# Optimization experiments

Measured on AMD Instinct MI355X. Metric: run time of the kernel, lower is better.

The kernel has to match this reference:

```python
import jax, jax.numpy as jnp
import numpy as np


def _conv2d(x, w, pad):
    return jax.lax.conv_general_dilated(
        x, w, (1, 1), [(pad, pad), (pad, pad)],
        dimension_numbers=('NCHW', 'OIHW', 'NCHW'))


def _affine_grid(theta, k):
    # torch F.affine_grid, align_corners=False; output size (k, k)
    base = ((2.0 * jnp.arange(k) + 1.0) / k - 1.0).astype(jnp.float32)
    pts = jnp.stack([
        jnp.broadcast_to(base[None, :], (k, k)),  # x varies along width
        jnp.broadcast_to(base[:, None], (k, k)),  # y varies along height
        jnp.ones((k, k), jnp.float32)], -1)        # [k,k,3]
    return jnp.einsum('ijc,nrc->nijr', pts, theta)  # [N,k,k,2] -> (x,y)


def _grid_sample(img, grid):
    # torch F.grid_sample: bilinear, zeros padding, align_corners=False
    # img [C,H,W], grid [k,k,2] with (x,y) in [-1,1]
    C, H, W = img.shape
    gx = (grid[..., 0] + 1.0) * W * 0.5 - 0.5
    gy = (grid[..., 1] + 1.0) * H * 0.5 - 0.5
    x0 = jnp.floor(gx); y0 = jnp.floor(gy)
    wx = gx - x0; wy = gy - y0
    x0i = x0.astype(jnp.int32); y0i = y0.astype(jnp.int32)

    def gath(yi, xi):
        valid = ((xi >= 0) & (xi < W) & (yi >= 0) & (yi < H)).astype(img.dtype)
        v = img[:, jnp.clip(yi, 0, H - 1), jnp.clip(xi, 0, W - 1)]  # [C,k,k]
        return v * valid[None]

    v00 = gath(y0i, x0i); v01 = gath(y0i, x0i + 1)
    v10 = gath(y0i + 1, x0i); v11 = gath(y0i + 1, x0i + 1)
    return (v00 * ((1 - wx) * (1 - wy))[None] + v01 * (wx * (1 - wy))[None]
            + v10 * ((1 - wx) * wy)[None] + v11 * (wx * wy)[None])


def reference(x, stn0_w, stn0_b, stn1_w, lin_w, lin_b, check):
    B, C, H, W = x.shape
    k = stn1_w.shape[-1]
    h = jax.nn.relu(_conv2d(x, stn0_w, k // 2) + stn0_b[None, :, None, None])
    ident6 = jnp.array([1., 0., 0., 0., 1., 0.], jnp.float32)
    out = _conv2d(h, stn1_w, 0) * (1.0 - check) + ident6[None, :, None, None]
    Ho, Wo = out.shape[2], out.shape[3]
    N = B * Ho * Wo
    # permute(0,3,2,1).view(N,2,3) as in torch
    theta = out.transpose(0, 3, 2, 1).reshape(N, 2, 3)
    grid = _affine_grid(theta, k)  # [N,k,k,2]
    xv = jnp.arange(k // 2, k // 2 + Ho, dtype=jnp.float32)[:, None]  # meshgrid 'ij'
    yv = jnp.arange(k // 2, k // 2 + Wo, dtype=jnp.float32)[None, :]
    half = float(k // 2)
    auxx = ((grid[..., 0] * half).reshape(B, Ho, Wo, k, k)
            + xv[None, :, :, None, None]).reshape(N, k, k) / (H - 1) * 2.0 - 1.0
    auxy = ((grid[..., 1] * half).reshape(B, Ho, Wo, k, k)
            + yv[None, :, :, None, None]).reshape(N, k, k) / (W - 1) * 2.0 - 1.0
    auxgrid = jnp.stack([auxx, auxy], -1).reshape(B, Ho * Wo, k, k, 2)
    # tile(x,0,Ho*Wo) duplicates x[b] for each of its Ho*Wo grids; gather directly
    xs = jax.vmap(lambda img, g: jax.vmap(lambda gg: _grid_sample(img, gg))(g))(x, auxgrid)  # [B,P,C,k,k]
    x_out = xs.reshape(N, -1) @ lin_w.T + lin_b  # [N,O]
    score = x_out.reshape(B, Ho, Wo, -1).transpose(0, 3, 2, 1)  # [B,O,Wo,Ho] as in torch
    ident23 = jnp.array([[1., 0., 0.], [0., 1., 0.]], jnp.float32)
    return score, ident23[None] - theta, out, auxx, auxy


def setup_inputs() -> dict:
    key = jax.random.key(0)
    ks = jax.random.split(key, 6)
    C, O, k = 128, 256, 3
    B, H, W = 8, 56, 56
    x = jax.random.normal(ks[0], (B, C, H, W), jnp.float32)
    stn0_w = jax.random.normal(ks[1], (C, C, k, k), jnp.float32) * (1.0 / np.sqrt(C * k * k))
    stn0_b = jax.random.normal(ks[2], (C,), jnp.float32) * 0.01
    # original zero-inits stn1; use small random so theta is non-trivial
    stn1_w = jax.random.normal(ks[3], (6, C, k, k), jnp.float32) * 0.01
    lin_w = jax.random.normal(ks[4], (O, C * k * k), jnp.float32) * (1.0 / np.sqrt(C * k * k))
    lin_b = jax.random.normal(ks[5], (O,), jnp.float32) * 0.01
    return {'x': x, 'stn0_w': stn0_w, 'stn0_b': stn0_b, 'stn1_w': stn1_w,
            'lin_w': lin_w, 'lin_b': lin_b, 'check': 0}
```

## Files before the change

kernel.cpp:

```cpp
#include <hip/hip_runtime.h>

typedef __attribute__((ext_vector_type(4))) float f32x4;
typedef __attribute__((ext_vector_type(8))) short bf16x8;

#define OPLANE 2916
#define NN 23328
#define KDIM 1152
#define PLANE 3136
#define LDP 72

__device__ __forceinline__ unsigned short f2bf(float f) {
    unsigned u = __builtin_bit_cast(unsigned, f);
    u += 0x7fffu + ((u >> 16) & 1u);
    return (unsigned short)(u >> 16);
}
__device__ __forceinline__ float bflo(unsigned u) {
    return __builtin_bit_cast(float, u << 16);
}
__device__ __forceinline__ float bfhi(unsigned u) {
    return __builtin_bit_cast(float, u & 0xffff0000u);
}

__global__ __launch_bounds__(256) void k_pre(const float* __restrict__ x,
                                             const float* __restrict__ w0,
                                             const float* __restrict__ lw,
                                             unsigned short* __restrict__ xnh,
                                             unsigned short* __restrict__ b1t,
                                             unsigned short* __restrict__ b2t) {
    __shared__ unsigned short lds[56 * 132];
    if (blockIdx.x < 1728) {
        int idx = blockIdx.x * 256 + threadIdx.x;
        if (idx < 147456) {
            int r = idx / KDIM, k = idx - r * KDIM;
            int ij = k >> 7, ic = k & 127;
            b1t[idx] = f2bf(w0[r * KDIM + ic * 9 + ij]);
        } else {
            int j = idx - 147456;
            int r = j / KDIM, k = j - r * KDIM;
            int ij = k >> 7, ic = k & 127;
            b2t[j] = f2bf(lw[r * KDIM + ic * 9 + ij]);
        }
    } else {
        const int bid = blockIdx.x - 1728;
        const int y = bid % 56, b = bid / 56, tid = threadIdx.x;
        for (int i = tid; i < 7168; i += 256) {
            int ic = i / 56, xc = i - ic * 56;
            lds[xc * 132 + ic] = f2bf(x[(b * 128 + ic) * PLANE + y * 56 + xc]);
        }
        __syncthreads();
        for (int i = tid; i < 7168; i += 256) {
            int xc = i >> 7, ic = i & 127;
            xnh[(b * PLANE + y * 56 + xc) * 128 + ic] = lds[xc * 132 + ic];
        }
    }
}

__global__ __launch_bounds__(512) void k_gemm1(const unsigned short* __restrict__ xnh,
                                               const unsigned short* __restrict__ Bt,
                                               const float* __restrict__ bias,
                                               unsigned short* __restrict__ h) {
    __shared__ unsigned short As[2][64 * LDP];
    __shared__ unsigned short Bs[2][128 * LDP];
    const int tid = threadIdx.x;
    const int lane = tid & 63, wid = tid >> 6;
    const int wr = wid >> 2, wc = wid & 3;
    const int mt_id = (blockIdx.x & 7) * 49 + (blockIdx.x >> 3);
    const int m0 = mt_id * 64;

    f32x4 acc[2][2];
    #pragma unroll
    for (int mt = 0; mt < 2; mt++)
        #pragma unroll
        for (int nt = 0; nt < 2; nt++) { acc[mt][nt][0]=0.f; acc[mt][nt][1]=0.f; acc[mt][nt][2]=0.f; acc[mt][nt][3]=0.f; }

    const int row = tid >> 3, q = tid & 7;
    const int p = m0 + row;
    const int b = p / PLANE; int rem = p - b * PLANE;
    const int y = rem / 56; const int xc = rem - y * 56;
    const int aswo = row * LDP + q * 8;
    const int brow = tid >> 2, bq = tid & 3;
    const unsigned short* bg = Bt + brow * KDIM + bq * 16;
    const int bswo = brow * LDP + bq * 16;
    const int lm = lane & 15, lq = lane >> 4;

    uint4 a0, bv0, bv1;
    auto issue = [&](int it) {
        const int ij = it >> 1;
        const int di = ij / 3, dj = ij - di * 3;
        const int icb = (it & 1) << 6;
        a0 = make_uint4(0u,0u,0u,0u);
        bool valid = (y + di >= 1) && (y + di <= 56) && (xc + dj >= 1) && (xc + dj <= 56);
        if (valid) {
            const unsigned short* ap = xnh + (p + (di - 1) * 56 + (dj - 1)) * 128 + icb + q * 8;
            a0 = *(const uint4*)ap;
        }
        bv0 = *(const uint4*)(bg + it * 64);
        bv1 = *(const uint4*)(bg + it * 64 + 8);
    };

    issue(0);
    *(uint4*)(&As[0][aswo]) = a0;
    *(uint4*)(&Bs[0][bswo + 0]) = bv0;
    *(uint4*)(&Bs[0][bswo + 8]) = bv1;
    __syncthreads();

    #pragma unroll
    for (int it = 0; it < 18; it++) {
        const int cur = it & 1;
        if (it < 17) issue(it + 1);
        #pragma unroll
        for (int kk = 0; kk < 64; kk += 32) {
            bf16x8 af[2], bf[2];
            #pragma unroll
            for (int mt = 0; mt < 2; mt++)
                af[mt] = *(const bf16x8*)&As[cur][(wr * 32 + mt * 16 + lm) * LDP + kk + lq * 8];
            #pragma unroll
            for (int nt = 0; nt < 2; nt++)
                bf[nt] = *(const bf16x8*)&Bs[cur][(wc * 32 + nt * 16 + lm) * LDP + kk + lq * 8];
            #pragma unroll
            for (int mt = 0; mt < 2; mt++)
                #pragma unroll
                for (int nt = 0; nt < 2; nt++)
                    acc[mt][nt] = __builtin_amdgcn_mfma_f32_16x16x32_bf16(af[mt], bf[nt], acc[mt][nt], 0, 0, 0);
        }
        if (it < 17) {
            const int nxt = cur ^ 1;
            *(uint4*)(&As[nxt][aswo]) = a0;
            *(uint4*)(&Bs[nxt][bswo + 0]) = bv0;
            *(uint4*)(&Bs[nxt][bswo + 8]) = bv1;
            __syncthreads();
        }
    }
    #pragma unroll
    for (int mt = 0; mt < 2; mt++) {
        int m = m0 + wr * 32 + mt * 16 + lq * 4;
        #pragma unroll
        for (int nt = 0; nt < 2; nt++) {
            int n = wc * 32 + nt * 16 + lm;
            float bb = bias[n];
            #pragma unroll
            for (int r = 0; r < 4; r++)
                h[(m + r) * 128 + n] = f2bf(fmaxf(acc[mt][nt][r] + bb, 0.f));
        }
    }
}

__global__ __launch_bounds__(256) void k_conv2f(const unsigned short* __restrict__ h,
                                                const float* __restrict__ w1,
                                                const int* __restrict__ check,
                                                float* __restrict__ o_out,
                                                float* __restrict__ o_th,
                                                float* __restrict__ o_ax,
                                                float* __restrict__ o_ay,
                                                float* __restrict__ sxy) {
    __shared__ float wlds[6912];
    __shared__ float red[16 * 6 * 17];
    __shared__ float vals[96];
    const int bid = (blockIdx.x & 7) * 183 + (blockIdx.x >> 3);
    if (bid >= 1458) return;
    const int tid = threadIdx.x;
    for (int idx = tid; idx < 6912; idx += 256) {
        int r = idx / KDIM, k = idx - r * KDIM;
        int ij = k >> 7, ic = k & 127;
        wlds[idx] = w1[r * KDIM + ic * 9 + ij];
    }
    __syncthreads();
    const int pt = tid >> 4, c = tid & 15;
    const int p = bid * 16 + pt;
    int b = p / OPLANE; int rem = p - b * OPLANE; int oh = rem / 54; int ow = rem - oh * 54;
    const uint4* h4 = (const uint4*)h;
    const float4* w4 = (const float4*)wlds;
    float acc[6] = {0.f, 0.f, 0.f, 0.f, 0.f, 0.f};
    const int base_sp = b * PLANE + oh * 56 + ow;
    #pragma unroll
    for (int i = 0; i < 3; i++) {
        #pragma unroll
        for (int j = 0; j < 3; j++) {
            int sp = base_sp + i * 56 + j;
            uint4 hu = h4[sp * 16 + c];
            float f0 = bflo(hu.x), f1 = bfhi(hu.x);
            float f2 = bflo(hu.y), f3 = bfhi(hu.y);
            float f4 = bflo(hu.z), f5 = bfhi(hu.z);
            float f6 = bflo(hu.w), f7 = bfhi(hu.w);
            int ij = i * 3 + j;
            #pragma unroll
            for (int r = 0; r < 6; r++) {
                float4 wa = w4[r * 288 + ij * 32 + c * 2];
                float4 wb = w4[r * 288 + ij * 32 + c * 2 + 1];
                acc[r] += f0 * wa.x + f1 * wa.y + f2 * wa.z + f3 * wa.w
                        + f4 * wb.x + f5 * wb.y + f6 * wb.z + f7 * wb.w;
            }
        }
    }
    #pragma unroll
    for (int r = 0; r < 6; r++) red[(pt * 6 + r) * 17 + c] = acc[r];
    __syncthreads();
    if (tid < 96) {
        const float* rp = &red[tid * 17];
        float s = 0.f;
        #pragma unroll
        for (int e = 0; e < 16; e++) s += rp[e];
        vals[tid] = s;
    }
    __syncthreads();
    if (tid < 16) {
        int p2 = bid * 16 + tid;
        int b2 = p2 / OPLANE; int r2 = p2 - b2 * OPLANE; int oh2 = r2 / 54; int ow2 = r2 - oh2 * 54;
        float val[6];
        float s = 1.0f - (float)check[0];
        const float id6[6] = {1.f, 0.f, 0.f, 0.f, 1.f, 0.f};
        #pragma unroll
        for (int r = 0; r < 6; r++) val[r] = vals[tid * 6 + r] * s + id6[r];
        int n = (b2 * 54 + ow2) * 54 + oh2;
        #pragma unroll
        for (int r = 0; r < 6; r++) {
            o_out[((b2 * 6 + r) * 54 + oh2) * 54 + ow2] = val[r];
            o_th[n * 6 + r] = id6[r] - val[r];
        }
        const float bse[3] = {-2.f / 3.f, 0.f, 2.f / 3.f};
        #pragma unroll
        for (int i = 0; i < 3; i++)
            #pragma unroll
            for (int j = 0; j < 3; j++) {
                float gx = bse[j] * val[0] + bse[i] * val[1] + val[2];
                float gy = bse[j] * val[3] + bse[i] * val[4] + val[5];
                float ax = (gx + 1.f + (float)ow2) * (2.f / 55.f) - 1.f;
                float ay = (gy + 1.f + (float)oh2) * (2.f / 55.f) - 1.f;
                int ij = i * 3 + j;
                o_ax[n * 9 + ij] = ax;
                o_ay[n * 9 + ij] = ay;
                sxy[(n * 9 + ij) * 2 + 0] = (ax + 1.f) * 28.f - 0.5f;
                sxy[(n * 9 + ij) * 2 + 1] = (ay + 1.f) * 28.f - 0.5f;
            }
    }
}

__global__ __launch_bounds__(256) void k_sgemm(const unsigned short* __restrict__ xnh,
                                               const unsigned short* __restrict__ Wt,
                                               const float* __restrict__ bias,
                                               const float* __restrict__ sxy,
                                               float* __restrict__ score) {
    __shared__ unsigned short Ss[64 * LDP];
    __shared__ unsigned short Ws[128 * LDP];
    const int i = blockIdx.x;
    const int xcd = i & 7, j = i >> 3;
    const int pp = xcd * 46 + (j >> 1);
    const int m8 = j & 1;
    if (pp >= 365) return;
    const int o0 = m8 * 128;
    const int s0 = pp * 64;
    const int tid = threadIdx.x;
    const int lane = tid & 63, wid = tid >> 6;
    const int wr = wid >> 1, wc = wid & 1;

    f32x4 acc[4][2];
    #pragma unroll
    for (int mt = 0; mt < 4; mt++)
        #pragma unroll
        for (int nt = 0; nt < 2; nt++) { acc[mt][nt][0]=0.f; acc[mt][nt][1]=0.f; acc[mt][nt][2]=0.f; acc[mt][nt][3]=0.f; }

    const int row = tid >> 2, q = tid & 3;
    const int mp = min(s0 + row, NN - 1);
    const int b = mp / OPLANE; const int rr = mp - b * OPLANE;
    const int ho = rr / 54, wo = rr - (rr / 54) * 54;
    const int n = (b * 54 + wo) * 54 + ho;
    const int xbase = b * PLANE;
    unsigned short* ssw = &Ss[row * LDP + q * 16];
    const int wrow = tid >> 1, wq = tid & 1;
    const unsigned short* wg = Wt + (o0 + wrow) * KDIM + wq * 32;
    unsigned short* wsw = &Ws[wrow * LDP + wq * 32];
    const int lm = lane & 15, lq = lane >> 4;

    float2 sc[9];
    {
        const float* spp = sxy + n * 18;
        #pragma unroll
        for (int ij = 0; ij < 9; ij++) sc[ij] = *(const float2*)(spp + ij * 2);
    }

    int off0 = 0, off1 = 0, off2 = 0, off3 = 0;
    float wt0 = 0.f, wt1 = 0.f, wt2 = 0.f, wt3 = 0.f;
    auto mkoff = [&](int ij) {
        float sx = sc[ij].x, sy = sc[ij].y;
        float x0f = floorf(sx), y0f = floorf(sy);
        float wx = sx - x0f, wy = sy - y0f;
        int x0 = (int)x0f, y0 = (int)y0f;
        int x1 = x0 + 1, y1 = y0 + 1;
        float vx0 = (x0 >= 0 && x0 < 56) ? 1.f : 0.f;
        float vx1 = (x1 >= 0 && x1 < 56) ? 1.f : 0.f;
        float vy0 = (y0 >= 0 && y0 < 56) ? 1.f : 0.f;
        float vy1 = (y1 >= 0 && y1 < 56) ? 1.f : 0.f;
        int xc0 = min(max(x0, 0), 55), xc1 = min(max(x1, 0), 55);
        int yc0 = min(max(y0, 0), 55), yc1 = min(max(y1, 0), 55);
        off0 = (xbase + yc0 * 56 + xc0) << 7;
        off1 = (xbase + yc0 * 56 + xc1) << 7;
        off2 = (xbase + yc1 * 56 + xc0) << 7;
        off3 = (xbase + yc1 * 56 + xc1) << 7;
        wt0 = vy0 * vx0 * (1.f - wx) * (1.f - wy);
        wt1 = vy0 * vx1 * wx * (1.f - wy);
        wt2 = vy1 * vx0 * (1.f - wx) * wy;
        wt3 = vy1 * vx1 * wx * wy;
    };

    uint4 p0a, p0b, p1a, p1b, p2a, p2b, p3a, p3b;
    uint4 w0v, w1v, w2v, w3v;
    auto issue = [&](int it) {
        const int co = ((it & 1) << 6) + q * 16;
        p0a = *(const uint4*)(xnh + off0 + co);
        p0b = *(const uint4*)(xnh + off0 + co + 8);
        p1a = *(const uint4*)(xnh + off1 + co);
        p1b = *(const uint4*)(xnh + off1 + co + 8);
        p2a = *(const uint4*)(xnh + off2 + co);
        p2b = *(const uint4*)(xnh + off2 + co + 8);
        p3a = *(const uint4*)(xnh + off3 + co);
        p3b = *(const uint4*)(xnh + off3 + co + 8);
        w0v = *(const uint4*)(wg + it * 64);
        w1v = *(const uint4*)(wg + it * 64 + 8);
        w2v = *(const uint4*)(wg + it * 64 + 16);
        w3v = *(const uint4*)(wg + it * 64 + 24);
    };

    mkoff(0);
    issue(0);

    #pragma unroll
    for (int it = 0; it < 18; it++) {
        unsigned dw[8];
        const unsigned* d0 = (const unsigned*)&p0a;
        const unsigned* d1 = (const unsigned*)&p1a;
        const unsigned* d2 = (const unsigned*)&p2a;
        const unsigned* d3 = (const unsigned*)&p3a;
        const unsigned* e0 = (const unsigned*)&p0b;
        const unsigned* e1 = (const unsigned*)&p1b;
        const unsigned* e2 = (const unsigned*)&p2b;
        const unsigned* e3 = (const unsigned*)&p3b;
        #pragma unroll
        for (int d = 0; d < 8; d++) {
            unsigned u0 = (d < 4) ? d0[d] : e0[d - 4];
            unsigned u1 = (d < 4) ? d1[d] : e1[d - 4];
            unsigned u2 = (d < 4) ? d2[d] : e2[d - 4];
            unsigned u3 = (d < 4) ? d3[d] : e3[d - 4];
            float lo = wt0 * bflo(u0) + wt1 * bflo(u1) + wt2 * bflo(u2) + wt3 * bflo(u3);
            float hi = wt0 * bfhi(u0) + wt1 * bfhi(u1) + wt2 * bfhi(u2) + wt3 * bfhi(u3);
            unsigned pk;
            asm("v_cvt_pk_bf16_f32 %0, %1, %2" : "=v"(pk) : "v"(lo), "v"(hi));
            dw[d] = pk;
        }
        __syncthreads();
        *(uint4*)(ssw + 0) = *(uint4*)&dw[0];
        *(uint4*)(ssw + 8) = *(uint4*)&dw[4];
        *(uint4*)(wsw + 0)  = w0v;
        *(uint4*)(wsw + 8)  = w1v;
        *(uint4*)(wsw + 16) = w2v;
        *(uint4*)(wsw + 24) = w3v;
        __syncthreads();
        if (it < 17) {
            if (((it + 1) & 1) == 0) mkoff((it + 1) >> 1);
            issue(it + 1);
        }
        #pragma unroll
        for (int kk = 0; kk < 64; kk += 32) {
            bf16x8 wf[4], sf[2];
            #pragma unroll
            for (int mt = 0; mt < 4; mt++)
                wf[mt] = *(const bf16x8*)&Ws[(wr * 64 + mt * 16 + lm) * LDP + kk + lq * 8];
            #pragma unroll
            for (int nt = 0; nt < 2; nt++)
                sf[nt] = *(const bf16x8*)&Ss[(wc * 32 + nt * 16 + lm) * LDP + kk + lq * 8];
            #pragma unroll
            for (int mt = 0; mt < 4; mt++)
                #pragma unroll
                for (int nt = 0; nt < 2; nt++)
                    acc[mt][nt] = __builtin_amdgcn_mfma_f32_16x16x32_bf16(wf[mt], sf[nt], acc[mt][nt], 0, 0, 0);
        }
    }
    #pragma unroll
    for (int mt = 0; mt < 4; mt++) {
        #pragma unroll
        for (int r = 0; r < 4; r++) {
            int o = o0 + wr * 64 + mt * 16 + lq * 4 + r;
            float bb = bias[o];
            #pragma unroll
            for (int nt = 0; nt < 2; nt++) {
                int s = s0 + wc * 32 + nt * 16 + lm;
                if (s < NN) {
                    int sb = s / OPLANE;
                    int soff = s - sb * OPLANE;
                    score[(sb * 256 + o) * OPLANE + soff] = acc[mt][nt][r] + bb;
                }
            }
        }
    }
}

extern "C" void kernel_launch(void* const* d_in, const int* in_sizes, int n_in,
                              void* d_out, int out_size, void* d_ws, size_t ws_size,
                              hipStream_t stream) {
    const float* x  = (const float*)d_in[0];
    const float* w0 = (const float*)d_in[1];
    const float* b0 = (const float*)d_in[2];
    const float* w1 = (const float*)d_in[3];
    const float* lw = (const float*)d_in[4];
    const float* lb = (const float*)d_in[5];
    const int* check = (const int*)d_in[6];

    float* out   = (float*)d_out;
    float* score = out;
    float* o_th  = out + 5971968;
    float* o_out = out + 6111936;
    float* o_ax  = out + 6251904;
    float* o_ay  = out + 6461856;

    char* wsb = (char*)d_ws;
    unsigned short* h   = (unsigned short*)wsb;
    unsigned short* xnh = (unsigned short*)(wsb + 12845056);
    unsigned short* b1t = (unsigned short*)(wsb + 19267584);
    unsigned short* b2t = (unsigned short*)(wsb + 19562496);
    float* sxy = (float*)(wsb + 20152320);

    k_pre<<<2176, 256, 0, stream>>>(x, w0, lw, xnh, b1t, b2t);
    k_gemm1<<<392, 512, 0, stream>>>(xnh, b1t, b0, h);
    k_conv2f<<<1464, 256, 0, stream>>>(h, w1, check, o_out, o_th, o_ax, o_ay, sxy);
    k_sgemm<<<736, 256, 0, stream>>>(xnh, b2t, lb, sxy, score);
}
```

Measured before the change: 160.3 us.

## Compute second conv on MFMA with bf16 weights padded to 16 rows

The 6-output-channel 3x3 conv that produces theta moves from per-thread fp32 dot products with a shared-memory reduction to a bf16 MFMA 16x16x32 GEMM over 64-pixel tiles. The weights are pre-converted to bf16 and zero-padded from 6 to 16 rows in the preprocessing kernel. This removes the fp32 weight staging and cross-thread reduction and cuts the block count. It spends MFMA work on the 10 padding rows and drops theta to bf16 weights, which could shift results slightly.

```diff
diff --git a/kernel.cpp b/kernel.cpp
--- a/kernel.cpp
+++ b/kernel.cpp
@@ -8,6 +8,7 @@
 #define KDIM 1152
 #define PLANE 3136
 #define LDP 72
+#define BS_LDP 1160
 
 __device__ __forceinline__ unsigned short f2bf(float f) {
     unsigned u = __builtin_bit_cast(unsigned, f);
@@ -24,9 +25,11 @@
 __global__ __launch_bounds__(256) void k_pre(const float* __restrict__ x,
                                              const float* __restrict__ w0,
                                              const float* __restrict__ lw,
+                                             const float* __restrict__ w1,
                                              unsigned short* __restrict__ xnh,
                                              unsigned short* __restrict__ b1t,
-                                             unsigned short* __restrict__ b2t) {
+                                             unsigned short* __restrict__ b2t,
+                                             unsigned short* __restrict__ b3t) {
     __shared__ unsigned short lds[56 * 132];
     if (blockIdx.x < 1728) {
         int idx = blockIdx.x * 256 + threadIdx.x;
@@ -40,8 +43,13 @@
             int ij = k >> 7, ic = k & 127;
             b2t[j] = f2bf(lw[r * KDIM + ic * 9 + ij]);
         }
+    } else if (blockIdx.x < 1800) {
+        int idx = (blockIdx.x - 1728) * 256 + threadIdx.x;
+        int r = idx / KDIM, k = idx - r * KDIM;
+        int ij = k >> 7, ic = k & 127;
+        b3t[idx] = (r < 6) ? f2bf(w1[r * KDIM + ic * 9 + ij]) : (unsigned short)0;
     } else {
-        const int bid = blockIdx.x - 1728;
+        const int bid = blockIdx.x - 1800;
         const int y = bid % 56, b = bid / 56, tid = threadIdx.x;
         for (int i = tid; i < 7168; i += 256) {
             int ic = i / 56, xc = i - ic * 56;
@@ -146,92 +154,106 @@
 }
 
 __global__ __launch_bounds__(256) void k_conv2f(const unsigned short* __restrict__ h,
-                                                const float* __restrict__ w1,
+                                                const unsigned short* __restrict__ Wt2,
                                                 const int* __restrict__ check,
                                                 float* __restrict__ o_out,
                                                 float* __restrict__ o_th,
                                                 float* __restrict__ o_ax,
                                                 float* __restrict__ o_ay,
                                                 float* __restrict__ sxy) {
-    __shared__ float wlds[6912];
-    __shared__ float red[16 * 6 * 17];
-    __shared__ float vals[96];
-    const int bid = (blockIdx.x & 7) * 183 + (blockIdx.x >> 3);
-    if (bid >= 1458) return;
+    __shared__ unsigned short Bs[16 * BS_LDP];
+    __shared__ unsigned short As[64 * LDP];
+    __shared__ float vals[64 * 6];
+    const int bid = (blockIdx.x & 7) * 46 + (blockIdx.x >> 3);
+    if (bid >= 365) return;
     const int tid = threadIdx.x;
-    for (int idx = tid; idx < 6912; idx += 256) {
-        int r = idx / KDIM, k = idx - r * KDIM;
-        int ij = k >> 7, ic = k & 127;
-        wlds[idx] = w1[r * KDIM + ic * 9 + ij];
+    const int lane = tid & 63, wid = tid >> 6;
+    const int lm = lane & 15, lq = lane >> 4;
+    const int m0 = bid * 64;
+
+    {
+        const int r = tid >> 4, kb = (tid & 15) * 72;
+        const unsigned short* src = Wt2 + r * KDIM + kb;
+        unsigned short* dst = &Bs[r * BS_LDP + kb];
+        #pragma unroll
+        for (int jj = 0; jj < 9; jj++)
+            *(uint4*)(dst + jj * 8) = *(const uint4*)(src + jj * 8);
+    }
+
+    const int row = tid >> 2, q = tid & 3;
+    const int p = min(m0 + row, NN - 1);
+    const int b = p / OPLANE; const int rr = p - b * OPLANE;
+    const int oh = rr / 54, ow = rr - oh * 54;
+    const int hbase = b * PLANE + oh * 56 + ow;
+    unsigned short* asw = &As[row * LDP + q * 16];
+
+    f32x4 acc; acc[0] = 0.f; acc[1] = 0.f; acc[2] = 0.f; acc[3] = 0.f;
+
+    uint4 a0, a1;
+    auto issue = [&](int it) {
+        const int ij = it >> 1;
+        const int di = ij / 3, dj = ij - di * 3;
+        const int icb = (it & 1) << 6;
+        const unsigned short* ap = h + (hbase + di * 56 + dj) * 128 + icb + q * 16;
+        a0 = *(const uint4*)ap;
+        a1 = *(const uint4*)(ap + 8);
+    };
+    issue(0);
+
+    #pragma unroll
+    for (int it = 0; it < 18; it++) {
+        __syncthreads();
+        *(uint4*)(asw + 0) = a0;
+        *(uint4*)(asw + 8) = a1;
+        __syncthreads();
+        if (it < 17) issue(it + 1);
+        #pragma unroll
+        for (int kk = 0; kk < 64; kk += 32) {
+            bf16x8 af = *(const bf16x8*)&As[(wid * 16 + lm) * LDP + kk + lq * 8];
+            bf16x8 bf = *(const bf16x8*)&Bs[lm * BS_LDP + it * 64 + kk + lq * 8];
+            acc = __builtin_amdgcn_mfma_f32_16x16x32_bf16(af, bf, acc, 0, 0, 0);
+        }
+    }
+
+    if (lm < 6) {
+        #pragma unroll
+        for (int r4 = 0; r4 < 4; r4++)
+            vals[(wid * 16 + lq * 4 + r4) * 6 + lm] = acc[r4];
     }
     __syncthreads();
-    const int pt = tid >> 4, c = tid & 15;
-    const int p = bid * 16 + pt;
-    int b = p / OPLANE; int rem = p - b * OPLANE; int oh = rem / 54; int ow = rem - oh * 54;
-    const uint4* h4 = (const uint4*)h;
-    const float4* w4 = (const float4*)wlds;
-    float acc[6] = {0.f, 0.f, 0.f, 0.f, 0.f, 0.f};
-    const int base_sp = b * PLANE + oh * 56 + ow;
-    #pragma unroll
-    for (int i = 0; i < 3; i++) {
-        #pragma unroll
-        for (int j = 0; j < 3; j++) {
-            int sp = base_sp + i * 56 + j;
-            uint4 hu = h4[sp * 16 + c];
-            float f0 = bflo(hu.x), f1 = bfhi(hu.x);
-            float f2 = bflo(hu.y), f3 = bfhi(hu.y);
-            float f4 = bflo(hu.z), f5 = bfhi(hu.z);
-            float f6 = bflo(hu.w), f7 = bfhi(hu.w);
-            int ij = i * 3 + j;
+
+    if (tid < 64) {
+        int p2 = m0 + tid;
+        if (p2 < NN) {
+            int b2 = p2 / OPLANE; int r2 = p2 - b2 * OPLANE;
+            int oh2 = r2 / 54; int ow2 = r2 - oh2 * 54;
+            float val[6];
+            float s = 1.0f - (float)check[0];
+            const float id6[6] = {1.f, 0.f, 0.f, 0.f, 1.f, 0.f};
+            #pragma unroll
+            for (int r = 0; r < 6; r++) val[r] = vals[tid * 6 + r] * s + id6[r];
+            int n = (b2 * 54 + ow2) * 54 + oh2;
             #pragma unroll
             for (int r = 0; r < 6; r++) {
-                float4 wa = w4[r * 288 + ij * 32 + c * 2];
-                float4 wb = w4[r * 288 + ij * 32 + c * 2 + 1];
-                acc[r] += f0 * wa.x + f1 * wa.y + f2 * wa.z + f3 * wa.w
-                        + f4 * wb.x + f5 * wb.y + f6 * wb.z + f7 * wb.w;
+                o_out[((b2 * 6 + r) * 54 + oh2) * 54 + ow2] = val[r];
+                o_th[n * 6 + r] = id6[r] - val[r];
             }
-        }
-    }
-    #pragma unroll
-    for (int r = 0; r < 6; r++) red[(pt * 6 + r) * 17 + c] = acc[r];
-    __syncthreads();
-    if (tid < 96) {
-        const float* rp = &red[tid * 17];
-        float s = 0.f;
-        #pragma unroll
-        for (int e = 0; e < 16; e++) s += rp[e];
-        vals[tid] = s;
-    }
-    __syncthreads();
-    if (tid < 16) {
-        int p2 = bid * 16 + tid;
-        int b2 = p2 / OPLANE; int r2 = p2 - b2 * OPLANE; int oh2 = r2 / 54; int ow2 = r2 - oh2 * 54;
-        float val[6];
-        float s = 1.0f - (float)check[0];
-        const float id6[6] = {1.f, 0.f, 0.f, 0.f, 1.f, 0.f};
-        #pragma unroll
-        for (int r = 0; r < 6; r++) val[r] = vals[tid * 6 + r] * s + id6[r];
-        int n = (b2 * 54 + ow2) * 54 + oh2;
-        #pragma unroll
-        for (int r = 0; r < 6; r++) {
-            o_out[((b2 * 6 + r) * 54 + oh2) * 54 + ow2] = val[r];
-            o_th[n * 6 + r] = id6[r] - val[r];
-        }
-        const float bse[3] = {-2.f / 3.f, 0.f, 2.f / 3.f};
-        #pragma unroll
-        for (int i = 0; i < 3; i++)
-            #pragma unroll
-            for (int j = 0; j < 3; j++) {
-                float gx = bse[j] * val[0] + bse[i] * val[1] + val[2];
-                float gy = bse[j] * val[3] + bse[i] * val[4] + val[5];
-                float ax = (gx + 1.f + (float)ow2) * (2.f / 55.f) - 1.f;
-                float ay = (gy + 1.f + (float)oh2) * (2.f / 55.f) - 1.f;
-                int ij = i * 3 + j;
-                o_ax[n * 9 + ij] = ax;
-                o_ay[n * 9 + ij] = ay;
-                sxy[(n * 9 + ij) * 2 + 0] = (ax + 1.f) * 28.f - 0.5f;
-                sxy[(n * 9 + ij) * 2 + 1] = (ay + 1.f) * 28.f - 0.5f;
-            }
+            const float bse[3] = {-2.f / 3.f, 0.f, 2.f / 3.f};
+            #pragma unroll
+            for (int i = 0; i < 3; i++)
+                #pragma unroll
+                for (int j = 0; j < 3; j++) {
+                    float gx = bse[j] * val[0] + bse[i] * val[1] + val[2];
+                    float gy = bse[j] * val[3] + bse[i] * val[4] + val[5];
+                    float ax = (gx + 1.f + (float)ow2) * (2.f / 55.f) - 1.f;
+                    float ay = (gy + 1.f + (float)oh2) * (2.f / 55.f) - 1.f;
+                    int ij = i * 3 + j;
+                    o_ax[n * 9 + ij] = ax;
+                    o_ay[n * 9 + ij] = ay;
+                    sxy[(n * 9 + ij) * 2 + 0] = (ax + 1.f) * 28.f - 0.5f;
+                    sxy[(n * 9 + ij) * 2 + 1] = (ay + 1.f) * 28.f - 0.5f;
+                }
+        }
     }
 }
 
@@ -413,13 +435,14 @@
 
     char* wsb = (char*)d_ws;
     unsigned short* h   = (unsigned short*)wsb;
+    unsigned short* b3t = (unsigned short*)(wsb + 6422528);
     unsigned short* xnh = (unsigned short*)(wsb + 12845056);
     unsigned short* b1t = (unsigned short*)(wsb + 19267584);
     unsigned short* b2t = (unsigned short*)(wsb + 19562496);
     float* sxy = (float*)(wsb + 20152320);
 
-    k_pre<<<2176, 256, 0, stream>>>(x, w0, lw, xnh, b1t, b2t);
+    k_pre<<<2248, 256, 0, stream>>>(x, w0, lw, w1, xnh, b1t, b2t, b3t);
     k_gemm1<<<392, 512, 0, stream>>>(xnh, b1t, b0, h);
-    k_conv2f<<<1464, 256, 0, stream>>>(h, w1, check, o_out, o_th, o_ax, o_ay, sxy);
+    k_conv2f<<<368, 256, 0, stream>>>(h, b3t, check, o_out, o_th, o_ax, o_ay, sxy);
     k_sgemm<<<736, 256, 0, stream>>>(xnh, b2t, lb, sxy, score);
 }
```

Result: faster. 154.8 us, median of 2 (-3.4%).
